# Kernel optimization log

Measured on AMD Instinct MI355X. Metric: run time of the kernel, lower is better.

Reference implementation:

```python
import jax, jax.numpy as jnp
import numpy as np

TEMP1 = 4.0  # local_temp1 default


def setup_inputs() -> dict:
    key = jax.random.key(0)
    k1, k2 = jax.random.split(key)
    query = jax.random.normal(k1, (256, 768, 96), dtype=jnp.float32)
    context = jax.random.normal(k2, (256, 768, 19, 19), dtype=jnp.float32)
    return {"query": query, "context": context}


def reference(query, context):
    # query: [B, ndf, Q]; context: [B, ndf, ih, iw]
    B, ndf, Q = query.shape
    ih, iw = context.shape[2], context.shape[3]
    S = ih * iw
    ctx = context.reshape(B, ndf, S)            # [B, ndf, S]
    # attn = contextT @ query -> [B, S, Q]
    attn = jnp.einsum('bds,bdq->bsq', ctx, query)
    # softmax over query dim
    attn = jax.nn.softmax(attn, axis=-1)
    # transpose to [B, Q, S], temperature scale, softmax over source dim
    attn = jnp.swapaxes(attn, 1, 2) * TEMP1
    attn = jax.nn.softmax(attn, axis=-1)        # [B, Q, S]
    # weightedContext = context @ attn^T -> [B, ndf, Q]
    weighted_context = jnp.einsum('bds,bqs->bdq', ctx, attn)
    attn_map = attn.reshape(B, Q, ih, iw)
    return weighted_context, attn_map
```

## Files before the change

### kernel.cpp

```cpp
#include <hip/hip_runtime.h>

#define NB 256
#define NDF 768
#define NQ 96
#define NS 361
#define LDT 36
#define LDP 392

typedef short bf16x4_t __attribute__((ext_vector_type(4)));
typedef short bf16x8_t __attribute__((ext_vector_type(8)));
typedef float f32x4_t __attribute__((ext_vector_type(4)));
typedef float f32x4u_t __attribute__((ext_vector_type(4), aligned(4)));
typedef unsigned int u32x2_t __attribute__((ext_vector_type(2)));
typedef unsigned int u32x4_t __attribute__((ext_vector_type(4)));

__device__ __forceinline__ unsigned pack_hi(unsigned u1, unsigned u0) {
    return __builtin_amdgcn_perm(u1, u0, 0x07060302u);
}

__device__ __forceinline__ bf16x8_t ld8(const unsigned short* p) {
    bf16x4_t a = *(const bf16x4_t*)p;
    bf16x4_t b = *(const bf16x4_t*)(p + 4);
    bf16x8_t r;
    r[0] = a[0]; r[1] = a[1]; r[2] = a[2]; r[3] = a[3];
    r[4] = b[0]; r[5] = b[1]; r[6] = b[2]; r[7] = b[3];
    return r;
}

__global__ __launch_bounds__(384, 3) void k1_gemm1_softmaxq(
    const float* __restrict__ Qg, const float* __restrict__ Cg, float* __restrict__ Aout)
{
    __shared__ unsigned short sQhi[NQ * LDT];
    __shared__ unsigned short sQlo[NQ * LDT];
    __shared__ unsigned short sShi[192 * LDT];
    __shared__ unsigned short sSlo[192 * LDT];

    const int b  = blockIdx.x >> 1;
    const int h  = blockIdx.x & 1;
    const int tid  = threadIdx.x;
    const int wv   = tid >> 6;
    const int lane = tid & 63;
    const int ll = lane & 15;
    const int lg = lane >> 4;
    const int s0 = 192 * h;

    const float* __restrict__ qg = Qg + (size_t)b * NDF * NQ;
    const float* __restrict__ cg = Cg + (size_t)b * NDF * NS;

    f32x4_t acc[6][2];
#pragma unroll
    for (int i = 0; i < 6; ++i)
#pragma unroll
        for (int j = 0; j < 2; ++j) acc[i][j] = (f32x4_t)0.0f;

    for (int k0 = 0; k0 < NDF; k0 += 32) {
        __syncthreads();
#pragma unroll
        for (int j = 0; j < 2; ++j) {
            int it = j * 384 + tid;
            int kq = it / NQ;
            int qq = it - kq * NQ;
            const float* p = qg + (k0 + 4 * kq) * NQ + qq;
            float x0 = p[0], x1 = p[NQ], x2 = p[2 * NQ], x3 = p[3 * NQ];
            unsigned u0 = __float_as_uint(x0), u1 = __float_as_uint(x1);
            unsigned u2 = __float_as_uint(x2), u3 = __float_as_uint(x3);
            float l0 = x0 - __uint_as_float(u0 & 0xFFFF0000u);
            float l1 = x1 - __uint_as_float(u1 & 0xFFFF0000u);
            float l2 = x2 - __uint_as_float(u2 & 0xFFFF0000u);
            float l3 = x3 - __uint_as_float(u3 & 0xFFFF0000u);
            u32x2_t hi, lo;
            hi[0] = pack_hi(u1, u0); hi[1] = pack_hi(u3, u2);
            lo[0] = pack_hi(__float_as_uint(l1), __float_as_uint(l0));
            lo[1] = pack_hi(__float_as_uint(l3), __float_as_uint(l2));
            int off = qq * LDT + 4 * kq;
            *(u32x2_t*)&sQhi[off] = hi;
            *(u32x2_t*)&sQlo[off] = lo;
        }
#pragma unroll
        for (int j = 0; j < 4; ++j) {
            int it = j * 384 + tid;
            int kq = it / 192;
            int ss = it - kq * 192;
            int s  = s0 + ss;
            bool ok = (s < NS);
            const float* p = cg + (k0 + 4 * kq) * NS + s;
            float x0 = ok ? p[0] : 0.0f;
            float x1 = ok ? p[NS] : 0.0f;
            float x2 = ok ? p[2 * NS] : 0.0f;
            float x3 = ok ? p[3 * NS] : 0.0f;
            unsigned u0 = __float_as_uint(x0), u1 = __float_as_uint(x1);
            unsigned u2 = __float_as_uint(x2), u3 = __float_as_uint(x3);
            float l0 = x0 - __uint_as_float(u0 & 0xFFFF0000u);
            float l1 = x1 - __uint_as_float(u1 & 0xFFFF0000u);
            float l2 = x2 - __uint_as_float(u2 & 0xFFFF0000u);
            float l3 = x3 - __uint_as_float(u3 & 0xFFFF0000u);
            u32x2_t hi, lo;
            hi[0] = pack_hi(u1, u0); hi[1] = pack_hi(u3, u2);
            lo[0] = pack_hi(__float_as_uint(l1), __float_as_uint(l0));
            lo[1] = pack_hi(__float_as_uint(l3), __float_as_uint(l2));
            int off = ss * LDT + 4 * kq;
            *(u32x2_t*)&sShi[off] = hi;
            *(u32x2_t*)&sSlo[off] = lo;
        }
        __syncthreads();

        bf16x8_t Bhi[2], Blo[2];
#pragma unroll
        for (int nt = 0; nt < 2; ++nt) {
            int row = 32 * wv + 16 * nt + ll;
            Bhi[nt] = ld8(&sShi[row * LDT + 8 * lg]);
            Blo[nt] = ld8(&sSlo[row * LDT + 8 * lg]);
        }
#pragma unroll
        for (int mt = 0; mt < 6; ++mt) {
            int row = 16 * mt + ll;
            bf16x8_t Ahi = ld8(&sQhi[row * LDT + 8 * lg]);
            bf16x8_t Alo = ld8(&sQlo[row * LDT + 8 * lg]);
#pragma unroll
            for (int nt = 0; nt < 2; ++nt) {
                acc[mt][nt] = __builtin_amdgcn_mfma_f32_16x16x32_bf16(Ahi, Bhi[nt], acc[mt][nt], 0, 0, 0);
                acc[mt][nt] = __builtin_amdgcn_mfma_f32_16x16x32_bf16(Ahi, Blo[nt], acc[mt][nt], 0, 0, 0);
                acc[mt][nt] = __builtin_amdgcn_mfma_f32_16x16x32_bf16(Alo, Bhi[nt], acc[mt][nt], 0, 0, 0);
            }
        }
    }

#pragma unroll
    for (int nt = 0; nt < 2; ++nt) {
        float m = -3.0e38f;
#pragma unroll
        for (int mt = 0; mt < 6; ++mt)
#pragma unroll
            for (int r = 0; r < 4; ++r) m = fmaxf(m, acc[mt][nt][r]);
        m = fmaxf(m, __shfl_xor(m, 16));
        m = fmaxf(m, __shfl_xor(m, 32));
        float sum = 0.0f;
#pragma unroll
        for (int mt = 0; mt < 6; ++mt)
#pragma unroll
            for (int r = 0; r < 4; ++r) {
                float e = __expf(acc[mt][nt][r] - m);
                acc[mt][nt][r] = e;
                sum += e;
            }
        sum += __shfl_xor(sum, 16);
        sum += __shfl_xor(sum, 32);
        float inv = 4.0f / sum;
#pragma unroll
        for (int mt = 0; mt < 6; ++mt)
#pragma unroll
            for (int r = 0; r < 4; ++r) acc[mt][nt][r] *= inv;
    }

    float* aout = Aout + (size_t)b * NQ * NS;
#pragma unroll
    for (int mt = 0; mt < 6; ++mt)
#pragma unroll
        for (int nt = 0; nt < 2; ++nt)
#pragma unroll
            for (int r = 0; r < 4; ++r) {
                int q = 16 * mt + 4 * lg + r;
                int s = s0 + 32 * wv + 16 * nt + ll;
                if (s < NS) aout[(size_t)q * NS + s] = acc[mt][nt][r];
            }
}

__global__ __launch_bounds__(256) void k15_softmaxs(float* __restrict__ Aout)
{
    const int b = blockIdx.x;
    const int q = blockIdx.y * 4 + (threadIdx.x >> 6);
    const int lane = threadIdx.x & 63;
    float* __restrict__ row = Aout + ((size_t)b * NQ + q) * NS;
    const int c0 = 6 * lane;

    float v[6];
    if (c0 + 5 < NS) {
        f32x4u_t t = *(const f32x4u_t*)(row + c0);
        v[0] = t[0]; v[1] = t[1]; v[2] = t[2]; v[3] = t[3];
        v[4] = row[c0 + 4]; v[5] = row[c0 + 5];
    } else {
#pragma unroll
        for (int i = 0; i < 6; ++i) v[i] = (c0 + i < NS) ? row[c0 + i] : -INFINITY;
    }
    float m = v[0];
#pragma unroll
    for (int i = 1; i < 6; ++i) m = fmaxf(m, v[i]);
#pragma unroll
    for (int o = 1; o < 64; o <<= 1) m = fmaxf(m, __shfl_xor(m, o));
    float e[6], sum = 0.0f;
#pragma unroll
    for (int i = 0; i < 6; ++i) { e[i] = __expf(v[i] - m); sum += e[i]; }
#pragma unroll
    for (int o = 1; o < 64; o <<= 1) sum += __shfl_xor(sum, o);
    float inv = 1.0f / sum;
    if (c0 + 5 < NS) {
        f32x4u_t t;
        t[0] = e[0] * inv; t[1] = e[1] * inv; t[2] = e[2] * inv; t[3] = e[3] * inv;
        *(f32x4u_t*)(row + c0) = t;
        row[c0 + 4] = e[4] * inv;
        row[c0 + 5] = e[5] * inv;
    } else {
#pragma unroll
        for (int i = 0; i < 6; ++i) if (c0 + i < NS) row[c0 + i] = e[i] * inv;
    }
}

__global__ __launch_bounds__(512, 4) void k3_gemm2(
    const float* __restrict__ Cg, const float* __restrict__ Aout, float* __restrict__ Wout)
{
    extern __shared__ char smem2[];
    unsigned short* sP = (unsigned short*)smem2;
    unsigned* sPd = (unsigned*)smem2;

    const int b = blockIdx.x >> 2;
    const int quarter = blockIdx.x & 3;
    const int tid  = threadIdx.x;
    const int wv   = tid >> 6;
    const int lane = tid & 63;
    const int ll = lane & 15;
    const int lg = lane >> 4;

    const float* __restrict__ attn = Aout + (size_t)b * NQ * NS;

    for (int i = tid; i < NQ * 181; i += 512) {
        int row = i / 181, p = i - row * 181;
        float x0 = attn[row * NS + 2 * p];
        float x1 = (p < 180) ? attn[row * NS + 2 * p + 1] : 0.0f;
        unsigned r0 = __float_as_uint(x0) + 0x8000u;
        unsigned r1 = __float_as_uint(x1) + 0x8000u;
        sPd[row * 196 + p] = pack_hi(r1, r0);
    }
    for (int i = tid; i < NQ * 15; i += 512) {
        int row = i / 15, p = i - row * 15;
        sPd[row * 196 + 181 + p] = 0;
    }
    __syncthreads();

    f32x4_t acc[3][3];
#pragma unroll
    for (int i = 0; i < 3; ++i)
#pragma unroll
        for (int j = 0; j < 3; ++j) acc[i][j] = (f32x4_t)0.0f;

    const float* __restrict__ cq = Cg + (size_t)b * NDF * NS + (size_t)(quarter * 192) * NS;
    const int dw = wv >> 1, qw = wv & 1;

#pragma unroll
    for (int c = 0; c < 12; ++c) {
        bf16x8_t Bf[3];
#pragma unroll
        for (int nt = 0; nt < 3; ++nt) {
            int row = 16 * (3 * qw + nt) + ll;
            Bf[nt] = *(const bf16x8_t*)&sP[row * LDP + 32 * c + 8 * lg];
        }
#pragma unroll
        for (int i = 0; i < 3; ++i) {
            int d = 16 * (3 * dw + i) + ll;
            const float* ap = cq + (size_t)d * NS + 32 * c + 8 * lg;
            u32x4_t u;
            if (c < 11) {
                f32x4u_t a0 = *(const f32x4u_t*)ap;
                f32x4u_t a1 = *(const f32x4u_t*)(ap + 4);
                u[0] = pack_hi(__float_as_uint(a0[1]), __float_as_uint(a0[0]));
                u[1] = pack_hi(__float_as_uint(a0[3]), __float_as_uint(a0[2]));
                u[2] = pack_hi(__float_as_uint(a1[1]), __float_as_uint(a1[0]));
                u[3] = pack_hi(__float_as_uint(a1[3]), __float_as_uint(a1[2]));
            } else {
                float t[8];
#pragma unroll
                for (int e = 0; e < 8; ++e) {
                    int s = 352 + 8 * lg + e;
                    t[e] = (s < NS) ? ap[e] : 0.0f;
                }
                u[0] = pack_hi(__float_as_uint(t[1]), __float_as_uint(t[0]));
                u[1] = pack_hi(__float_as_uint(t[3]), __float_as_uint(t[2]));
                u[2] = pack_hi(__float_as_uint(t[5]), __float_as_uint(t[4]));
                u[3] = pack_hi(__float_as_uint(t[7]), __float_as_uint(t[6]));
            }
            bf16x8_t Af = __builtin_bit_cast(bf16x8_t, u);
#pragma unroll
            for (int nt = 0; nt < 3; ++nt)
                acc[i][nt] = __builtin_amdgcn_mfma_f32_16x16x32_bf16(Af, Bf[nt], acc[i][nt], 0, 0, 0);
        }
    }

    float* wout = Wout + (size_t)b * NDF * NQ;
#pragma unroll
    for (int i = 0; i < 3; ++i)
#pragma unroll
        for (int nt = 0; nt < 3; ++nt)
#pragma unroll
            for (int r = 0; r < 4; ++r) {
                int d = quarter * 192 + 16 * (3 * dw + i) + 4 * lg + r;
                int q = 16 * (3 * qw + nt) + ll;
                wout[(size_t)d * NQ + q] = acc[i][nt][r];
            }
}

extern "C" void kernel_launch(void* const* d_in, const int* in_sizes, int n_in,
                              void* d_out, int out_size, void* d_ws, size_t ws_size,
                              hipStream_t stream) {
    const float* Qg = (const float*)d_in[0];
    const float* Cg = (const float*)d_in[1];
    float* Wout = (float*)d_out;
    float* Aout = Wout + (size_t)NB * NDF * NQ;

    hipLaunchKernelGGL(k1_gemm1_softmaxq, dim3(NB * 2), dim3(384), 0, stream, Qg, Cg, Aout);
    hipLaunchKernelGGL(k15_softmaxs, dim3(NB, 24), dim3(256), 0, stream, Aout);
    (void)hipFuncSetAttribute((const void*)k3_gemm2,
                              hipFuncAttributeMaxDynamicSharedMemorySize, NQ * LDP * 2);
    hipLaunchKernelGGL(k3_gemm2, dim3(NB * 4), dim3(512), NQ * LDP * 2, stream, Cg, Aout, Wout);
}
```

Baseline: 253.5 us.

## Fuse source-dim softmax into gemm2 via bf16 workspace and register-prefetch gemm1

Gemm1 now prefetches the next K-slice of query and context into registers while MFMAs run on the current slice, and pads the LDS stride to 40 for aligned 16-byte fragment loads. When a workspace is available, gemm1 writes its scaled attention as bf16 into the workspace instead of fp32. Gemm2 then computes the source-dim softmax in shared memory, applies the normalisation to its output, and only one quarter-block writes the fp32 attention map. This removes the separate softmax kernel and a full fp32 round trip of the attention map, at the cost of redundant softmax work in each of the four gemm2 blocks per batch and bf16 rounding before the exponent.

Measured after the change: 229.4 us. 1.11x faster.

```diff
diff --git a/kernel.cpp b/kernel.cpp
--- a/kernel.cpp
+++ b/kernel.cpp
@@ -4,45 +4,53 @@
 #define NDF 768
 #define NQ 96
 #define NS 361
-#define LDT 36
+#define LDT 40
 #define LDP 392
-
-typedef short bf16x4_t __attribute__((ext_vector_type(4)));
+#define WSROW 368
+#define WS_BYTES ((size_t)NB * NQ * WSROW * 2)
+
 typedef short bf16x8_t __attribute__((ext_vector_type(8)));
 typedef float f32x4_t __attribute__((ext_vector_type(4)));
 typedef float f32x4u_t __attribute__((ext_vector_type(4), aligned(4)));
 typedef unsigned int u32x2_t __attribute__((ext_vector_type(2)));
 typedef unsigned int u32x4_t __attribute__((ext_vector_type(4)));
 
-__device__ __forceinline__ unsigned pack_hi(unsigned u1, unsigned u0) {
-    return __builtin_amdgcn_perm(u1, u0, 0x07060302u);
-}
-
-__device__ __forceinline__ bf16x8_t ld8(const unsigned short* p) {
-    bf16x4_t a = *(const bf16x4_t*)p;
-    bf16x4_t b = *(const bf16x4_t*)(p + 4);
-    bf16x8_t r;
-    r[0] = a[0]; r[1] = a[1]; r[2] = a[2]; r[3] = a[3];
-    r[4] = b[0]; r[5] = b[1]; r[6] = b[2]; r[7] = b[3];
-    return r;
-}
-
+__device__ __forceinline__ unsigned pack_hi(unsigned b_, unsigned a_) {
+    return __builtin_amdgcn_perm(b_, a_, 0x07060302u);
+}
+__device__ __forceinline__ unsigned short f2bf(float x) {
+    unsigned u = __float_as_uint(x);
+    u += 0x7FFFu + ((u >> 16) & 1u);
+    return (unsigned short)(u >> 16);
+}
+__device__ __forceinline__ float bf2f(unsigned short h) {
+    return __uint_as_float(((unsigned)h) << 16);
+}
+
+template<bool WSP>
 __global__ __launch_bounds__(384, 3) void k1_gemm1_softmaxq(
-    const float* __restrict__ Qg, const float* __restrict__ Cg, float* __restrict__ Aout)
+    const float* __restrict__ Qg, const float* __restrict__ Cg,
+    unsigned short* __restrict__ Wsb, float* __restrict__ AoutF)
 {
     __shared__ unsigned short sQhi[NQ * LDT];
     __shared__ unsigned short sQlo[NQ * LDT];
     __shared__ unsigned short sShi[192 * LDT];
     __shared__ unsigned short sSlo[192 * LDT];
 
-    const int b  = blockIdx.x >> 1;
-    const int h  = blockIdx.x & 1;
-    const int tid  = threadIdx.x;
-    const int wv   = tid >> 6;
+    const int b = blockIdx.x >> 1;
+    const int h = blockIdx.x & 1;
+    const int tid = threadIdx.x;
+    const int wv = tid >> 6;
     const int lane = tid & 63;
     const int ll = lane & 15;
     const int lg = lane >> 4;
     const int s0 = 192 * h;
+    const int qq  = tid % NQ;
+    const int kqQ = tid / NQ;
+    const int ssb = tid % 192;
+    const int kqC = tid / 192;
+    const int sAbs = s0 + ssb;
+    const bool okC = (sAbs < NS);
 
     const float* __restrict__ qg = Qg + (size_t)b * NDF * NQ;
     const float* __restrict__ cg = Cg + (size_t)b * NDF * NS;
@@ -53,77 +61,91 @@
 #pragma unroll
         for (int j = 0; j < 2; ++j) acc[i][j] = (f32x4_t)0.0f;
 
-    for (int k0 = 0; k0 < NDF; k0 += 32) {
-        __syncthreads();
-#pragma unroll
-        for (int j = 0; j < 2; ++j) {
-            int it = j * 384 + tid;
-            int kq = it / NQ;
-            int qq = it - kq * NQ;
-            const float* p = qg + (k0 + 4 * kq) * NQ + qq;
-            float x0 = p[0], x1 = p[NQ], x2 = p[2 * NQ], x3 = p[3 * NQ];
-            unsigned u0 = __float_as_uint(x0), u1 = __float_as_uint(x1);
-            unsigned u2 = __float_as_uint(x2), u3 = __float_as_uint(x3);
-            float l0 = x0 - __uint_as_float(u0 & 0xFFFF0000u);
-            float l1 = x1 - __uint_as_float(u1 & 0xFFFF0000u);
-            float l2 = x2 - __uint_as_float(u2 & 0xFFFF0000u);
-            float l3 = x3 - __uint_as_float(u3 & 0xFFFF0000u);
-            u32x2_t hi, lo;
-            hi[0] = pack_hi(u1, u0); hi[1] = pack_hi(u3, u2);
-            lo[0] = pack_hi(__float_as_uint(l1), __float_as_uint(l0));
-            lo[1] = pack_hi(__float_as_uint(l3), __float_as_uint(l2));
-            int off = qq * LDT + 4 * kq;
-            *(u32x2_t*)&sQhi[off] = hi;
-            *(u32x2_t*)&sQlo[off] = lo;
-        }
-#pragma unroll
-        for (int j = 0; j < 4; ++j) {
-            int it = j * 384 + tid;
-            int kq = it / 192;
-            int ss = it - kq * 192;
-            int s  = s0 + ss;
-            bool ok = (s < NS);
-            const float* p = cg + (k0 + 4 * kq) * NS + s;
-            float x0 = ok ? p[0] : 0.0f;
-            float x1 = ok ? p[NS] : 0.0f;
-            float x2 = ok ? p[2 * NS] : 0.0f;
-            float x3 = ok ? p[3 * NS] : 0.0f;
-            unsigned u0 = __float_as_uint(x0), u1 = __float_as_uint(x1);
-            unsigned u2 = __float_as_uint(x2), u3 = __float_as_uint(x3);
-            float l0 = x0 - __uint_as_float(u0 & 0xFFFF0000u);
-            float l1 = x1 - __uint_as_float(u1 & 0xFFFF0000u);
-            float l2 = x2 - __uint_as_float(u2 & 0xFFFF0000u);
-            float l3 = x3 - __uint_as_float(u3 & 0xFFFF0000u);
-            u32x2_t hi, lo;
-            hi[0] = pack_hi(u1, u0); hi[1] = pack_hi(u3, u2);
-            lo[0] = pack_hi(__float_as_uint(l1), __float_as_uint(l0));
-            lo[1] = pack_hi(__float_as_uint(l3), __float_as_uint(l2));
-            int off = ss * LDT + 4 * kq;
-            *(u32x2_t*)&sShi[off] = hi;
-            *(u32x2_t*)&sSlo[off] = lo;
-        }
-        __syncthreads();
-
-        bf16x8_t Bhi[2], Blo[2];
-#pragma unroll
-        for (int nt = 0; nt < 2; ++nt) {
-            int row = 32 * wv + 16 * nt + ll;
-            Bhi[nt] = ld8(&sShi[row * LDT + 8 * lg]);
-            Blo[nt] = ld8(&sSlo[row * LDT + 8 * lg]);
-        }
-#pragma unroll
-        for (int mt = 0; mt < 6; ++mt) {
-            int row = 16 * mt + ll;
-            bf16x8_t Ahi = ld8(&sQhi[row * LDT + 8 * lg]);
-            bf16x8_t Alo = ld8(&sQlo[row * LDT + 8 * lg]);
-#pragma unroll
-            for (int nt = 0; nt < 2; ++nt) {
-                acc[mt][nt] = __builtin_amdgcn_mfma_f32_16x16x32_bf16(Ahi, Bhi[nt], acc[mt][nt], 0, 0, 0);
-                acc[mt][nt] = __builtin_amdgcn_mfma_f32_16x16x32_bf16(Ahi, Blo[nt], acc[mt][nt], 0, 0, 0);
-                acc[mt][nt] = __builtin_amdgcn_mfma_f32_16x16x32_bf16(Alo, Bhi[nt], acc[mt][nt], 0, 0, 0);
-            }
-        }
-    }
+    float RQa[8], RCa[16], RQb[8], RCb[16];
+
+#define LOADQ(K0, R) { \
+    const float* p = qg + ((K0) + 4 * kqQ) * NQ + qq; \
+    R[0] = p[0]; R[1] = p[NQ]; R[2] = p[2 * NQ]; R[3] = p[3 * NQ]; \
+    const float* p2 = p + 16 * NQ; \
+    R[4] = p2[0]; R[5] = p2[NQ]; R[6] = p2[2 * NQ]; R[7] = p2[3 * NQ]; }
+
+#define LOADC(K0, R) { \
+    const float* p = cg + ((K0) + 4 * kqC) * NS + sAbs; \
+    _Pragma("unroll") \
+    for (int j = 0; j < 4; ++j) { \
+        const float* pj = p + j * 8 * NS; \
+        R[4*j+0] = okC ? pj[0] : 0.0f; \
+        R[4*j+1] = okC ? pj[NS] : 0.0f; \
+        R[4*j+2] = okC ? pj[2*NS] : 0.0f; \
+        R[4*j+3] = okC ? pj[3*NS] : 0.0f; } }
+
+#define STOREQC(RQ, RC) { \
+    _Pragma("unroll") \
+    for (int t = 0; t < 2; ++t) { \
+        unsigned u0 = __float_as_uint(RQ[4*t+0]), u1 = __float_as_uint(RQ[4*t+1]); \
+        unsigned u2 = __float_as_uint(RQ[4*t+2]), u3 = __float_as_uint(RQ[4*t+3]); \
+        float l0 = RQ[4*t+0] - __uint_as_float(u0 & 0xFFFF0000u); \
+        float l1 = RQ[4*t+1] - __uint_as_float(u1 & 0xFFFF0000u); \
+        float l2 = RQ[4*t+2] - __uint_as_float(u2 & 0xFFFF0000u); \
+        float l3 = RQ[4*t+3] - __uint_as_float(u3 & 0xFFFF0000u); \
+        u32x2_t hi, lo; \
+        hi[0] = pack_hi(u1, u0); hi[1] = pack_hi(u3, u2); \
+        lo[0] = pack_hi(__float_as_uint(l1), __float_as_uint(l0)); \
+        lo[1] = pack_hi(__float_as_uint(l3), __float_as_uint(l2)); \
+        int off = qq * LDT + 4 * (kqQ + 4 * t); \
+        *(u32x2_t*)&sQhi[off] = hi; \
+        *(u32x2_t*)&sQlo[off] = lo; } \
+    _Pragma("unroll") \
+    for (int j = 0; j < 4; ++j) { \
+        unsigned u0 = __float_as_uint(RC[4*j+0]), u1 = __float_as_uint(RC[4*j+1]); \
+        unsigned u2 = __float_as_uint(RC[4*j+2]), u3 = __float_as_uint(RC[4*j+3]); \
+        float l0 = RC[4*j+0] - __uint_as_float(u0 & 0xFFFF0000u); \
+        float l1 = RC[4*j+1] - __uint_as_float(u1 & 0xFFFF0000u); \
+        float l2 = RC[4*j+2] - __uint_as_float(u2 & 0xFFFF0000u); \
+        float l3 = RC[4*j+3] - __uint_as_float(u3 & 0xFFFF0000u); \
+        u32x2_t hi, lo; \
+        hi[0] = pack_hi(u1, u0); hi[1] = pack_hi(u3, u2); \
+        lo[0] = pack_hi(__float_as_uint(l1), __float_as_uint(l0)); \
+        lo[1] = pack_hi(__float_as_uint(l3), __float_as_uint(l2)); \
+        int off = ssb * LDT + 4 * (kqC + 2 * j); \
+        *(u32x2_t*)&sShi[off] = hi; \
+        *(u32x2_t*)&sSlo[off] = lo; } }
+
+#define FRAGMFMA() { \
+    bf16x8_t Bhi[2], Blo[2]; \
+    _Pragma("unroll") \
+    for (int nt = 0; nt < 2; ++nt) { \
+        int row = 32 * wv + 16 * nt + ll; \
+        Bhi[nt] = *(const bf16x8_t*)&sShi[row * LDT + 8 * lg]; \
+        Blo[nt] = *(const bf16x8_t*)&sSlo[row * LDT + 8 * lg]; } \
+    _Pragma("unroll") \
+    for (int mt = 0; mt < 6; ++mt) { \
+        int row = 16 * mt + ll; \
+        bf16x8_t Ahi = *(const bf16x8_t*)&sQhi[row * LDT + 8 * lg]; \
+        bf16x8_t Alo = *(const bf16x8_t*)&sQlo[row * LDT + 8 * lg]; \
+        _Pragma("unroll") \
+        for (int nt = 0; nt < 2; ++nt) { \
+            acc[mt][nt] = __builtin_amdgcn_mfma_f32_16x16x32_bf16(Ahi, Bhi[nt], acc[mt][nt], 0, 0, 0); \
+            acc[mt][nt] = __builtin_amdgcn_mfma_f32_16x16x32_bf16(Ahi, Blo[nt], acc[mt][nt], 0, 0, 0); \
+            acc[mt][nt] = __builtin_amdgcn_mfma_f32_16x16x32_bf16(Alo, Bhi[nt], acc[mt][nt], 0, 0, 0); } } }
+
+    LOADQ(0, RQa); LOADC(0, RCa);
+    for (int k0 = 0; k0 < NDF; k0 += 64) {
+        STOREQC(RQa, RCa);
+        __syncthreads();
+        if (k0 + 32 < NDF) { LOADQ(k0 + 32, RQb); LOADC(k0 + 32, RCb); }
+        FRAGMFMA();
+        __syncthreads();
+        STOREQC(RQb, RCb);
+        __syncthreads();
+        if (k0 + 64 < NDF) { LOADQ(k0 + 64, RQa); LOADC(k0 + 64, RCa); }
+        FRAGMFMA();
+        __syncthreads();
+    }
+#undef LOADQ
+#undef LOADC
+#undef STOREQC
+#undef FRAGMFMA
 
 #pragma unroll
     for (int nt = 0; nt < 2; ++nt) {
@@ -152,17 +174,31 @@
             for (int r = 0; r < 4; ++r) acc[mt][nt][r] *= inv;
     }
 
-    float* aout = Aout + (size_t)b * NQ * NS;
-#pragma unroll
-    for (int mt = 0; mt < 6; ++mt)
-#pragma unroll
-        for (int nt = 0; nt < 2; ++nt)
-#pragma unroll
-            for (int r = 0; r < 4; ++r) {
-                int q = 16 * mt + 4 * lg + r;
-                int s = s0 + 32 * wv + 16 * nt + ll;
-                if (s < NS) aout[(size_t)q * NS + s] = acc[mt][nt][r];
-            }
+    if constexpr (WSP) {
+        unsigned short* wr = Wsb + (size_t)b * NQ * WSROW;
+#pragma unroll
+        for (int mt = 0; mt < 6; ++mt)
+#pragma unroll
+            for (int nt = 0; nt < 2; ++nt)
+#pragma unroll
+                for (int r = 0; r < 4; ++r) {
+                    int q = 16 * mt + 4 * lg + r;
+                    int s = s0 + 32 * wv + 16 * nt + ll;
+                    if (s < NS) wr[q * WSROW + s] = f2bf(acc[mt][nt][r]);
+                }
+    } else {
+        float* aout = AoutF + (size_t)b * NQ * NS;
+#pragma unroll
+        for (int mt = 0; mt < 6; ++mt)
+#pragma unroll
+            for (int nt = 0; nt < 2; ++nt)
+#pragma unroll
+                for (int r = 0; r < 4; ++r) {
+                    int q = 16 * mt + 4 * lg + r;
+                    int s = s0 + 32 * wv + 16 * nt + ll;
+                    if (s < NS) aout[(size_t)q * NS + s] = acc[mt][nt][r];
+                }
+    }
 }
 
 __global__ __launch_bounds__(256) void k15_softmaxs(float* __restrict__ Aout)
@@ -193,48 +229,111 @@
 #pragma unroll
     for (int o = 1; o < 64; o <<= 1) sum += __shfl_xor(sum, o);
     float inv = 1.0f / sum;
-    if (c0 + 5 < NS) {
-        f32x4u_t t;
-        t[0] = e[0] * inv; t[1] = e[1] * inv; t[2] = e[2] * inv; t[3] = e[3] * inv;
-        *(f32x4u_t*)(row + c0) = t;
-        row[c0 + 4] = e[4] * inv;
-        row[c0 + 5] = e[5] * inv;
-    } else {
-#pragma unroll
-        for (int i = 0; i < 6; ++i) if (c0 + i < NS) row[c0 + i] = e[i] * inv;
-    }
-}
-
-__global__ __launch_bounds__(512, 4) void k3_gemm2(
-    const float* __restrict__ Cg, const float* __restrict__ Aout, float* __restrict__ Wout)
+#pragma unroll
+    for (int i = 0; i < 6; ++i) if (c0 + i < NS) row[c0 + i] = e[i] * inv;
+}
+
+template<bool FUSED>
+__global__ __launch_bounds__(512, 4) void k2_gemm2(
+    const float* __restrict__ Cg, const unsigned short* __restrict__ Wsb,
+    const float* __restrict__ AttnF, float* __restrict__ Wout, float* __restrict__ AoutF)
 {
     extern __shared__ char smem2[];
     unsigned short* sP = (unsigned short*)smem2;
     unsigned* sPd = (unsigned*)smem2;
+    float* sMax = (float*)(smem2 + NQ * LDP * 2);
+    float* sInv = sMax + NQ;
 
     const int b = blockIdx.x >> 2;
     const int quarter = blockIdx.x & 3;
-    const int tid  = threadIdx.x;
-    const int wv   = tid >> 6;
+    const int tid = threadIdx.x;
+    const int wv = tid >> 6;
     const int lane = tid & 63;
     const int ll = lane & 15;
     const int lg = lane >> 4;
 
-    const float* __restrict__ attn = Aout + (size_t)b * NQ * NS;
-
-    for (int i = tid; i < NQ * 181; i += 512) {
-        int row = i / 181, p = i - row * 181;
-        float x0 = attn[row * NS + 2 * p];
-        float x1 = (p < 180) ? attn[row * NS + 2 * p + 1] : 0.0f;
-        unsigned r0 = __float_as_uint(x0) + 0x8000u;
-        unsigned r1 = __float_as_uint(x1) + 0x8000u;
-        sPd[row * 196 + p] = pack_hi(r1, r0);
-    }
-    for (int i = tid; i < NQ * 15; i += 512) {
-        int row = i / 15, p = i - row * 15;
-        sPd[row * 196 + 181 + p] = 0;
-    }
-    __syncthreads();
+    if constexpr (FUSED) {
+        const unsigned* __restrict__ wsd = (const unsigned*)(Wsb + (size_t)b * NQ * WSROW);
+        for (int i = tid; i < NQ * 184; i += 512) {
+            int r = i / 184, c = i - r * 184;
+            sPd[r * 196 + c] = wsd[i];
+        }
+        for (int i = tid; i < NQ * 12; i += 512) {
+            int r = i / 12, c = i - r * 12;
+            sPd[r * 196 + 184 + c] = 0;
+        }
+        __syncthreads();
+
+        const int l32 = tid & 31;
+        const int rbase = tid >> 5;
+#pragma unroll
+        for (int pass = 0; pass < 6; ++pass) {
+            int row = pass * 16 + rbase;
+            float m = -3.0e38f;
+#pragma unroll
+            for (int j = 0; j < 6; ++j) {
+                int dw = l32 + 32 * j;
+                if (dw < 184) {
+                    unsigned u = sPd[row * 196 + dw];
+                    float v0 = bf2f((unsigned short)(u & 0xFFFFu));
+                    float v1 = bf2f((unsigned short)(u >> 16));
+                    if (2 * dw < NS) m = fmaxf(m, v0);
+                    if (2 * dw + 1 < NS) m = fmaxf(m, v1);
+                }
+            }
+#pragma unroll
+            for (int o = 1; o < 32; o <<= 1) m = fmaxf(m, __shfl_xor(m, o));
+            if (l32 == 0) sMax[row] = m;
+        }
+        __syncthreads();
+#pragma unroll
+        for (int pass = 0; pass < 6; ++pass) {
+            int row = pass * 16 + rbase;
+            float m = sMax[row];
+            float sum = 0.0f;
+#pragma unroll
+            for (int j = 0; j < 6; ++j) {
+                int dw = l32 + 32 * j;
+                if (dw < 184) {
+                    unsigned u = sPd[row * 196 + dw];
+                    float v0 = bf2f((unsigned short)(u & 0xFFFFu));
+                    float v1 = bf2f((unsigned short)(u >> 16));
+                    float e0 = (2 * dw < NS) ? __expf(v0 - m) : 0.0f;
+                    float e1 = (2 * dw + 1 < NS) ? __expf(v1 - m) : 0.0f;
+                    sum += e0 + e1;
+                    sPd[row * 196 + dw] = ((unsigned)f2bf(e1) << 16) | (unsigned)f2bf(e0);
+                }
+            }
+#pragma unroll
+            for (int o = 1; o < 32; o <<= 1) sum += __shfl_xor(sum, o);
+            if (l32 == 0) sInv[row] = sum;
+        }
+        __syncthreads();
+        if (tid < NQ) sInv[tid] = 1.0f / sInv[tid];
+        __syncthreads();
+        if (quarter == 0) {
+            float* aout = AoutF + (size_t)b * NQ * NS;
+            for (int i = tid; i < NQ * NS; i += 512) {
+                int q = i / NS, s = i - q * NS;
+                aout[i] = bf2f(sP[q * LDP + s]) * sInv[q];
+            }
+        }
+    } else {
+        const float* __restrict__ attn = AttnF + (size_t)b * NQ * NS;
+        for (int i = tid; i < NQ * 181; i += 512) {
+            int row = i / 181, p = i - row * 181;
+            float x0 = attn[row * NS + 2 * p];
+            float x1 = (p < 180) ? attn[row * NS + 2 * p + 1] : 0.0f;
+            unsigned r0 = __float_as_uint(x0) + 0x8000u;
+            unsigned r1 = __float_as_uint(x1) + 0x8000u;
+            sPd[row * 196 + p] = pack_hi(r1, r0);
+        }
+        for (int i = tid; i < NQ * 15; i += 512) {
+            int row = i / 15, p = i - row * 15;
+            sPd[row * 196 + 181 + p] = 0;
+        }
+        __syncthreads();
+    }
 
     f32x4_t acc[3][3];
 #pragma unroll
@@ -285,6 +384,12 @@
     }
 
     float* wout = Wout + (size_t)b * NDF * NQ;
+    float invq[3];
+#pragma unroll
+    for (int nt = 0; nt < 3; ++nt) {
+        if constexpr (FUSED) invq[nt] = sInv[16 * (3 * qw + nt) + ll];
+        else invq[nt] = 1.0f;
+    }
 #pragma unroll
     for (int i = 0; i < 3; ++i)
 #pragma unroll
@@ -293,7 +398,7 @@
             for (int r = 0; r < 4; ++r) {
                 int d = quarter * 192 + 16 * (3 * dw + i) + 4 * lg + r;
                 int q = 16 * (3 * qw + nt) + ll;
-                wout[(size_t)d * NQ + q] = acc[i][nt][r];
+                wout[(size_t)d * NQ + q] = acc[i][nt][r] * invq[nt];
             }
 }
 
@@ -305,9 +410,19 @@
     float* Wout = (float*)d_out;
     float* Aout = Wout + (size_t)NB * NDF * NQ;
 
-    hipLaunchKernelGGL(k1_gemm1_softmaxq, dim3(NB * 2), dim3(384), 0, stream, Qg, Cg, Aout);
-    hipLaunchKernelGGL(k15_softmaxs, dim3(NB, 24), dim3(256), 0, stream, Aout);
-    (void)hipFuncSetAttribute((const void*)k3_gemm2,
-                              hipFuncAttributeMaxDynamicSharedMemorySize, NQ * LDP * 2);
-    hipLaunchKernelGGL(k3_gemm2, dim3(NB * 4), dim3(512), NQ * LDP * 2, stream, Cg, Aout, Wout);
-}
+    const int smem2 = NQ * LDP * 2 + NQ * 8;
+
+    if (ws_size >= WS_BYTES) {
+        unsigned short* wsb = (unsigned short*)d_ws;
+        k1_gemm1_softmaxq<true><<<dim3(NB * 2), dim3(384), 0, stream>>>(Qg, Cg, wsb, nullptr);
+        (void)hipFuncSetAttribute((const void*)k2_gemm2<true>,
+                                  hipFuncAttributeMaxDynamicSharedMemorySize, smem2);
+        k2_gemm2<true><<<dim3(NB * 4), dim3(512), smem2, stream>>>(Cg, wsb, nullptr, Wout, Aout);
+    } else {
+        k1_gemm1_softmaxq<false><<<dim3(NB * 2), dim3(384), 0, stream>>>(Qg, Cg, nullptr, Aout);
+        k15_softmaxs<<<dim3(NB, 24), dim3(256), 0, stream>>>(Aout);
+        (void)hipFuncSetAttribute((const void*)k2_gemm2<false>,
+                                  hipFuncAttributeMaxDynamicSharedMemorySize, smem2);
+        k2_gemm2<false><<<dim3(NB * 4), dim3(512), smem2, stream>>>(Cg, nullptr, Aout, Wout, Aout);
+    }
+}
```
